# Kernel optimization log

Hardware: AMD Instinct MI355X
Metric: run time of the kernel (lower is better)

The kernel has to match this reference:

```python
import jax, jax.numpy as jnp
import numpy as np

N, HW, L = 16, 3136, 64
C_IN, C_OUT, D = 256, 512, 256


def setup_inputs() -> dict:
    key = jax.random.key(0)
    ks = jax.random.split(key, 8)
    # xavier-normal-ish scale for weights
    def xav(k, shape):
        fan_in, fan_out = shape[1], shape[0]
        std = (2.0 / (fan_in + fan_out)) ** 0.5
        return jax.random.normal(k, shape, dtype=jnp.float32) * std
    return {
        "x": jax.random.normal(ks[0], (N, HW, C_IN), dtype=jnp.float32),
        "t": jax.random.normal(ks[1], (N, L, D), dtype=jnp.float32),
        "W1": xav(ks[2], (D, C_IN)),      # linear1 weight (out,in), no bias
        "W2": xav(ks[3], (D, D)),         # linear2 weight, no bias
        "W3": xav(ks[4], (C_OUT, D)),     # linear3 weight
        "b3": jnp.zeros((C_OUT,), dtype=jnp.float32),
        "Wd": xav(ks[5], (C_OUT, C_IN)),  # downsample weight
        "bd": jnp.zeros((C_OUT,), dtype=jnp.float32),
    }


def reference(x, t, W1, W2, W3, b3, Wd, bd):
    # x: (N, HW, C_in), t: (N, L, D)
    x_q = jnp.einsum("npc,dc->npd", x, W1)          # (N, HW, D)
    t_q = jnp.einsum("nld,ed->nle", t, W2)          # (N, L, D)
    a = jnp.einsum("npd,nld->npl", x_q, t_q)        # unscaled QK^T (N, HW, L)
    a = jax.nn.softmax(a, axis=2)
    t3 = jnp.einsum("nld,od->nlo", t, W3) + b3      # (N, L, C_out)
    av = jnp.einsum("npl,nlo->npo", a, t3)          # (N, HW, C_out)
    x_ds = jnp.einsum("npc,oc->npo", x, Wd) + bd    # downsample residual
    return x_ds + av
```

## Files before the change

kernel.cpp:

```cpp
#include <hip/hip_runtime.h>


typedef unsigned short u16;
using half8 = __attribute__((ext_vector_type(8))) _Float16;
using f32x4 = __attribute__((ext_vector_type(4))) float;

__device__ __forceinline__ u16 f2h(float f) {
  _Float16 h = (_Float16)f;
  union { _Float16 h; u16 u; } cv; cv.h = h;
  return cv.u;
}

__device__ __forceinline__ f32x4 mfma16(half8 a, half8 b, f32x4 c) {
  return __builtin_amdgcn_mfma_f32_16x16x32_f16(a, b, c, 0, 0, 0);
}

__global__ __launch_bounds__(256) void reblock_kernel(
    const float* __restrict__ W1, const float* __restrict__ W2,
    const float* __restrict__ W3, const float* __restrict__ Wd,
    const float* __restrict__ t,
    u16* __restrict__ W1f, u16* __restrict__ W2f, u16* __restrict__ W3f,
    u16* __restrict__ Wdf, u16* __restrict__ tf) {
  int b = blockIdx.x, k = threadIdx.x;
  const float* src; u16* dst; int row;
  if (b < 256)       { src = W1; dst = W1f; row = b; }
  else if (b < 512)  { src = W2; dst = W2f; row = b - 256; }
  else if (b < 1024) { src = W3; dst = W3f; row = b - 512; }
  else if (b < 1536) { src = Wd; dst = Wdf; row = b - 1024; }
  else               { src = t;  dst = tf;  row = b - 1536; }
  float v = src[(size_t)row*256 + k];
  int flat = ((row >> 4)*8 + (k >> 5))*512 + ((k >> 3) & 3)*128 + (row & 15)*8 + (k & 7);
  dst[flat] = f2h(v);
}

__global__ __launch_bounds__(256) void tq_t3t_kernel(
    const u16* __restrict__ tf, const u16* __restrict__ W2f,
    const u16* __restrict__ W3f, const float* __restrict__ b3,
    u16* __restrict__ tqf, u16* __restrict__ t3f) {
  const int tid = threadIdx.x, w = tid >> 6, lane = tid & 63;
  const int quad = lane >> 4, l16 = lane & 15;
  const int b = blockIdx.x;

  if (b < 64) {
    const int n = b >> 2, eb = b & 3;
    const int gW2 = eb*4 + w;
    f32x4 acc[4];
    #pragma unroll
    for (int mt = 0; mt < 4; ++mt) acc[mt] = (f32x4){0.f, 0.f, 0.f, 0.f};
    #pragma unroll
    for (int kc = 0; kc < 8; ++kc) {
      half8 bf = *(const half8*)(W2f + (gW2*8 + kc)*512 + lane*8);
      #pragma unroll
      for (int mt = 0; mt < 4; ++mt) {
        half8 a = *(const half8*)(tf + ((n*4 + mt)*8 + kc)*512 + lane*8);
        acc[mt] = mfma16(a, bf, acc[mt]);
      }
    }
    #pragma unroll
    for (int mt = 0; mt < 4; ++mt)
      #pragma unroll
      for (int r = 0; r < 4; ++r) {
        int flat = ((n*4 + mt)*8 + eb*2 + (w >> 1))*512
                 + ((w & 1)*2 + (l16 >> 3))*128 + (quad*4 + r)*8 + (l16 & 7);
        tqf[flat] = f2h(acc[mt][r]);
      }
  } else {
    const int b2 = b - 64;
    const int n = b2 >> 3, ob = b2 & 7;
    const int gW3 = ob*4 + w;
    f32x4 acc[4];
    #pragma unroll
    for (int nt = 0; nt < 4; ++nt) acc[nt] = (f32x4){0.f, 0.f, 0.f, 0.f};
    #pragma unroll
    for (int kc = 0; kc < 8; ++kc) {
      half8 a = *(const half8*)(W3f + (gW3*8 + kc)*512 + lane*8);
      #pragma unroll
      for (int nt = 0; nt < 4; ++nt) {
        half8 bf = *(const half8*)(tf + ((n*4 + nt)*8 + kc)*512 + lane*8);
        acc[nt] = mfma16(a, bf, acc[nt]);
      }
    }
    #pragma unroll
    for (int nt = 0; nt < 4; ++nt)
      #pragma unroll
      for (int r = 0; r < 4; ++r) {
        int o = ob*64 + w*16 + quad*4 + r;
        int flat = ((n*32 + ob*4 + w)*2 + (nt >> 1))*512
                 + ((nt & 1)*2 + (l16 >> 3))*128 + (quad*4 + r)*8 + (l16 & 7);
        t3f[flat] = f2h(acc[nt][r] + b3[o]);
      }
  }
}

__global__ __launch_bounds__(512, 4) void main_kernel(
    const float* __restrict__ x, const u16* __restrict__ W1f,
    const u16* __restrict__ Wdf, const u16* __restrict__ tqf,
    const u16* __restrict__ t3f, const float* __restrict__ bd,
    float* __restrict__ out) {
  __shared__ __attribute__((aligned(16))) char smem[34816 + 17408];
  u16* xs   = (u16*)smem;
  u16* pool = (u16*)(smem + 34816);

  const int bid = blockIdx.x;
  const int n = bid / 49;
  const int pt = bid - n*49;
  const int m0 = pt * 64;
  const int tid = threadIdx.x, w = tid >> 6, lane = tid & 63;
  const int quad = lane >> 4, l16 = lane & 15;

  half8 w1a[8];
  {
    const u16* p = W1f + (size_t)w*8*512;
    #pragma unroll
    for (int kc = 0; kc < 8; ++kc) w1a[kc] = *(const half8*)(p + kc*512 + lane*8);
  }
  float bias[4];
  #pragma unroll
  for (int ot = 0; ot < 4; ++ot) bias[ot] = bd[w*64 + ot*16 + l16];

  {
    const float4* xg = (const float4*)(x + (size_t)(n*3136 + m0)*256);
    #pragma unroll
    for (int it = 0; it < 8; ++it) {
      int idx = it*512 + tid;
      int r = idx >> 6, c4 = idx & 63;
      float4 v = xg[idx];
      ushort4 u;
      u.x = f2h(v.x); u.y = f2h(v.y); u.z = f2h(v.z); u.w = f2h(v.w);
      *(ushort4*)(&xs[r*264 + c4*4]) = u;
    }
  }
  __syncthreads();

  f32x4 acc1[4];
  #pragma unroll
  for (int mt = 0; mt < 4; ++mt) acc1[mt] = (f32x4){0.f, 0.f, 0.f, 0.f};
  #pragma unroll
  for (int kc = 0; kc < 8; ++kc)
    #pragma unroll
    for (int mt = 0; mt < 4; ++mt) {
      half8 a = *(const half8*)(&xs[(mt*16 + l16)*264 + kc*32 + quad*8]);
      acc1[mt] = mfma16(a, w1a[kc], acc1[mt]);
    }
  #pragma unroll
  for (int mt = 0; mt < 4; ++mt)
    #pragma unroll
    for (int r = 0; r < 4; ++r)
      pool[(mt*16 + quad*4 + r)*136 + w*16 + l16] = f2h(acc1[mt][r]);
  __syncthreads();

  f32x4 acc2[4];
  #pragma unroll
  for (int lt = 0; lt < 4; ++lt) acc2[lt] = (f32x4){0.f, 0.f, 0.f, 0.f};
  f32x4 acc[4][4];
  #pragma unroll
  for (int mt = 0; mt < 4; ++mt)
    #pragma unroll
    for (int ot = 0; ot < 4; ++ot) acc[mt][ot] = (f32x4){0.f, 0.f, 0.f, 0.f};

  f32x4 acc1b[4];
  #pragma unroll
  for (int mt = 0; mt < 4; ++mt) acc1b[mt] = (f32x4){0.f, 0.f, 0.f, 0.f};
  {
    const u16* p = W1f + (size_t)(8 + w)*8*512;
    #pragma unroll
    for (int kc = 0; kc < 8; ++kc) {
      half8 bf = *(const half8*)(p + kc*512 + lane*8);
      #pragma unroll
      for (int mt = 0; mt < 4; ++mt) {
        half8 a = *(const half8*)(&xs[(mt*16 + l16)*264 + kc*32 + quad*8]);
        acc1b[mt] = mfma16(a, bf, acc1b[mt]);
      }
    }
  }
  if (w < 4) {
    #pragma unroll
    for (int k2 = 0; k2 < 4; ++k2) {
      half8 a = *(const half8*)(&pool[(w*16 + l16)*136 + k2*32 + quad*8]);
      #pragma unroll
      for (int lt = 0; lt < 4; ++lt) {
        half8 bf = *(const half8*)(tqf + ((n*4 + lt)*8 + 0*4 + k2)*512 + lane*8);
        acc2[lt] = mfma16(a, bf, acc2[lt]);
      }
    }
  }
  __syncthreads();
  #pragma unroll
  for (int mt = 0; mt < 4; ++mt)
    #pragma unroll
    for (int r = 0; r < 4; ++r)
      pool[(mt*16 + quad*4 + r)*136 + w*16 + l16] = f2h(acc1b[mt][r]);
  __syncthreads();

  if (w < 4) {
    #pragma unroll
    for (int k2 = 0; k2 < 4; ++k2) {
      half8 a = *(const half8*)(&pool[(w*16 + l16)*136 + k2*32 + quad*8]);
      #pragma unroll
      for (int lt = 0; lt < 4; ++lt) {
        half8 bf = *(const half8*)(tqf + ((n*4 + lt)*8 + 1*4 + k2)*512 + lane*8);
        acc2[lt] = mfma16(a, bf, acc2[lt]);
      }
    }
  }
  #pragma unroll
  for (int kc = 0; kc < 8; ++kc) {
    half8 a[4];
    #pragma unroll
    for (int mt = 0; mt < 4; ++mt)
      a[mt] = *(const half8*)(&xs[(mt*16 + l16)*264 + kc*32 + quad*8]);
    #pragma unroll
    for (int ot = 0; ot < 4; ++ot) {
      half8 bf = *(const half8*)(Wdf + ((w*4 + ot)*8 + kc)*512 + lane*8);
      #pragma unroll
      for (int mt = 0; mt < 4; ++mt) acc[mt][ot] = mfma16(a[mt], bf, acc[mt][ot]);
    }
  }
  __syncthreads();

  if (w < 4) {
    #pragma unroll
    for (int r = 0; r < 4; ++r) {
      float s0 = acc2[0][r], s1 = acc2[1][r], s2 = acc2[2][r], s3 = acc2[3][r];
      float mx = fmaxf(fmaxf(s0, s1), fmaxf(s2, s3));
      #pragma unroll
      for (int off = 8; off >= 1; off >>= 1) mx = fmaxf(mx, __shfl_xor(mx, off, 64));
      float e0 = __expf(s0 - mx), e1 = __expf(s1 - mx);
      float e2 = __expf(s2 - mx), e3 = __expf(s3 - mx);
      float s = e0 + e1 + e2 + e3;
      #pragma unroll
      for (int off = 8; off >= 1; off >>= 1) s += __shfl_xor(s, off, 64);
      float inv = 1.0f / s;
      int row = (w*16 + quad*4 + r)*72;
      pool[row +  0 + l16] = f2h(e0 * inv);
      pool[row + 16 + l16] = f2h(e1 * inv);
      pool[row + 32 + l16] = f2h(e2 * inv);
      pool[row + 48 + l16] = f2h(e3 * inv);
    }
  }
  __syncthreads();

  #pragma unroll
  for (int kc3 = 0; kc3 < 2; ++kc3) {
    half8 a[4];
    #pragma unroll
    for (int mt = 0; mt < 4; ++mt)
      a[mt] = *(const half8*)(&pool[(mt*16 + l16)*72 + kc3*32 + quad*8]);
    #pragma unroll
    for (int ot = 0; ot < 4; ++ot) {
      half8 bf = *(const half8*)(t3f + ((n*32 + w*4 + ot)*2 + kc3)*512 + lane*8);
      #pragma unroll
      for (int mt = 0; mt < 4; ++mt) acc[mt][ot] = mfma16(a[mt], bf, acc[mt][ot]);
    }
  }

  float* sc = (float*)smem + w*1088;
  #pragma unroll
  for (int mt = 0; mt < 4; ++mt) {
    #pragma unroll
    for (int ot = 0; ot < 4; ++ot)
      #pragma unroll
      for (int r = 0; r < 4; ++r)
        sc[(quad*4 + r)*68 + ot*16 + l16] = acc[mt][ot][r] + bias[ot];
    #pragma unroll
    for (int i = 0; i < 4; ++i) {
      float4 v = *(float4*)&sc[(i*4 + quad)*68 + l16*4];
      *(float4*)&out[(size_t)(n*3136 + m0 + mt*16 + i*4 + quad)*512 + w*64 + l16*4] = v;
    }
  }
}

extern "C" void kernel_launch(void* const* d_in, const int* in_sizes, int n_in,
                              void* d_out, int out_size, void* d_ws, size_t ws_size,
                              hipStream_t stream) {
  const float* x  = (const float*)d_in[0];
  const float* t  = (const float*)d_in[1];
  const float* W1 = (const float*)d_in[2];
  const float* W2 = (const float*)d_in[3];
  const float* W3 = (const float*)d_in[4];
  const float* b3 = (const float*)d_in[5];
  const float* Wd = (const float*)d_in[6];
  const float* bd = (const float*)d_in[7];
  float* out = (float*)d_out;

  char* ws = (char*)d_ws;
  u16* W1f = (u16*)(ws + 0);
  u16* W2f = (u16*)(ws + 131072);
  u16* W3f = (u16*)(ws + 262144);
  u16* Wdf = (u16*)(ws + 524288);
  u16* tf  = (u16*)(ws + 786432);
  u16* tqf = (u16*)(ws + 1310720);
  u16* t3f = (u16*)(ws + 1835008);

  hipLaunchKernelGGL(reblock_kernel, dim3(2560), dim3(256), 0, stream,
                     W1, W2, W3, Wd, t, W1f, W2f, W3f, Wdf, tf);
  hipLaunchKernelGGL(tq_t3t_kernel, dim3(192), dim3(256), 0, stream,
                     tf, W2f, W3f, b3, tqf, t3f);
  hipLaunchKernelGGL(main_kernel, dim3(784), dim3(512), 0, stream,
                     x, W1f, Wdf, tqf, t3f, bd, out);
}
```

Baseline: 196.2 us.

## Halve main kernel tile to 32 rows with 4 waves and split softmax

The main kernel now processes 32 pixel rows per block with 256 threads instead of 64 rows with 512, doubling the grid to 1568 blocks. Each wave computes two W1 column tiles and 128 output columns, done in two halves so fewer accumulators are live at once. The softmax over L is split across wave pairs and combined through a small shared buffer of partial max and sum values, so all waves take part instead of half. Output is stored straight from registers without the shared-memory staging pass. This gives more blocks and less shared memory per block, at the cost of less reuse of weight fragments per pixel, more global weight traffic, and uncoalesced output stores.

```diff
diff --git a/kernel.cpp b/kernel.cpp
--- a/kernel.cpp
+++ b/kernel.cpp
@@ -92,37 +92,41 @@
   }
 }
 
-__global__ __launch_bounds__(512, 4) void main_kernel(
+__global__ __launch_bounds__(256, 4) void main_kernel(
     const float* __restrict__ x, const u16* __restrict__ W1f,
     const u16* __restrict__ Wdf, const u16* __restrict__ tqf,
     const u16* __restrict__ t3f, const float* __restrict__ bd,
     float* __restrict__ out) {
-  __shared__ __attribute__((aligned(16))) char smem[34816 + 17408];
-  u16* xs   = (u16*)smem;
-  u16* pool = (u16*)(smem + 34816);
+  __shared__ __attribute__((aligned(16))) char smem[34816];
+  u16* xs  = (u16*)smem;
+  u16* xq0 = (u16*)(smem + 16896);
+  u16* xq1 = (u16*)(smem + 25600);
+  float* parts = (float*)(smem + 34304);
 
   const int bid = blockIdx.x;
-  const int n = bid / 49;
-  const int pt = bid - n*49;
-  const int m0 = pt * 64;
+  const int n  = bid / 98;
+  const int pt = bid - n*98;
+  const int m0 = pt * 32;
   const int tid = threadIdx.x, w = tid >> 6, lane = tid & 63;
   const int quad = lane >> 4, l16 = lane & 15;
+  const int rb = w & 1;
+  const int lh = w >> 1;
 
   half8 w1a[8];
   {
-    const u16* p = W1f + (size_t)w*8*512;
+    const u16* p = W1f + (size_t)(w*2)*8*512;
     #pragma unroll
     for (int kc = 0; kc < 8; ++kc) w1a[kc] = *(const half8*)(p + kc*512 + lane*8);
   }
-  float bias[4];
-  #pragma unroll
-  for (int ot = 0; ot < 4; ++ot) bias[ot] = bd[w*64 + ot*16 + l16];
+  float bias[8];
+  #pragma unroll
+  for (int og = 0; og < 8; ++og) bias[og] = bd[w*128 + og*16 + l16];
 
   {
     const float4* xg = (const float4*)(x + (size_t)(n*3136 + m0)*256);
     #pragma unroll
     for (int it = 0; it < 8; ++it) {
-      int idx = it*512 + tid;
+      int idx = it*256 + tid;
       int r = idx >> 6, c4 = idx & 63;
       float4 v = xg[idx];
       ushort4 u;
@@ -132,142 +136,187 @@
   }
   __syncthreads();
 
-  f32x4 acc1[4];
-  #pragma unroll
-  for (int mt = 0; mt < 4; ++mt) acc1[mt] = (f32x4){0.f, 0.f, 0.f, 0.f};
-  #pragma unroll
-  for (int kc = 0; kc < 8; ++kc)
-    #pragma unroll
-    for (int mt = 0; mt < 4; ++mt) {
-      half8 a = *(const half8*)(&xs[(mt*16 + l16)*264 + kc*32 + quad*8]);
-      acc1[mt] = mfma16(a, w1a[kc], acc1[mt]);
-    }
-  #pragma unroll
-  for (int mt = 0; mt < 4; ++mt)
-    #pragma unroll
-    for (int r = 0; r < 4; ++r)
-      pool[(mt*16 + quad*4 + r)*136 + w*16 + l16] = f2h(acc1[mt][r]);
-  __syncthreads();
-
-  f32x4 acc2[4];
-  #pragma unroll
-  for (int lt = 0; lt < 4; ++lt) acc2[lt] = (f32x4){0.f, 0.f, 0.f, 0.f};
-  f32x4 acc[4][4];
-  #pragma unroll
-  for (int mt = 0; mt < 4; ++mt)
+  f32x4 acc1[2][2];
+  #pragma unroll
+  for (int i = 0; i < 2; ++i)
+    #pragma unroll
+    for (int mt = 0; mt < 2; ++mt) acc1[i][mt] = (f32x4){0.f, 0.f, 0.f, 0.f};
+  {
+    const u16* p1 = W1f + (size_t)(w*2 + 1)*8*512;
+    #pragma unroll
+    for (int kc = 0; kc < 8; ++kc) {
+      half8 a0 = *(const half8*)(&xs[(l16)*264 + kc*32 + quad*8]);
+      half8 a1 = *(const half8*)(&xs[(16 + l16)*264 + kc*32 + quad*8]);
+      acc1[0][0] = mfma16(a0, w1a[kc], acc1[0][0]);
+      acc1[0][1] = mfma16(a1, w1a[kc], acc1[0][1]);
+      half8 bf = *(const half8*)(p1 + kc*512 + lane*8);
+      acc1[1][0] = mfma16(a0, bf, acc1[1][0]);
+      acc1[1][1] = mfma16(a1, bf, acc1[1][1]);
+    }
+  }
+  #pragma unroll
+  for (int i = 0; i < 2; ++i)
+    #pragma unroll
+    for (int mt = 0; mt < 2; ++mt)
+      #pragma unroll
+      for (int r = 0; r < 4; ++r)
+        xq0[(mt*16 + quad*4 + r)*136 + (w*2 + i)*16 + l16] = f2h(acc1[i][mt][r]);
+  __syncthreads();
+
+  f32x4 acc2[2];
+  acc2[0] = (f32x4){0.f, 0.f, 0.f, 0.f};
+  acc2[1] = (f32x4){0.f, 0.f, 0.f, 0.f};
+  #pragma unroll
+  for (int k2 = 0; k2 < 4; ++k2) {
+    half8 a = *(const half8*)(&xq0[(rb*16 + l16)*136 + k2*32 + quad*8]);
+    #pragma unroll
+    for (int j = 0; j < 2; ++j) {
+      half8 bf = *(const half8*)(tqf + ((size_t)(n*4 + lh*2 + j)*8 + k2)*512 + lane*8);
+      acc2[j] = mfma16(a, bf, acc2[j]);
+    }
+  }
+  {
+    f32x4 acc1b[2][2];
+    #pragma unroll
+    for (int i = 0; i < 2; ++i)
+      #pragma unroll
+      for (int mt = 0; mt < 2; ++mt) acc1b[i][mt] = (f32x4){0.f, 0.f, 0.f, 0.f};
+    const u16* pa = W1f + (size_t)(8 + w*2)*8*512;
+    const u16* pb = W1f + (size_t)(9 + w*2)*8*512;
+    #pragma unroll
+    for (int kc = 0; kc < 8; ++kc) {
+      half8 a0 = *(const half8*)(&xs[(l16)*264 + kc*32 + quad*8]);
+      half8 a1 = *(const half8*)(&xs[(16 + l16)*264 + kc*32 + quad*8]);
+      half8 bfA = *(const half8*)(pa + kc*512 + lane*8);
+      half8 bfB = *(const half8*)(pb + kc*512 + lane*8);
+      acc1b[0][0] = mfma16(a0, bfA, acc1b[0][0]);
+      acc1b[0][1] = mfma16(a1, bfA, acc1b[0][1]);
+      acc1b[1][0] = mfma16(a0, bfB, acc1b[1][0]);
+      acc1b[1][1] = mfma16(a1, bfB, acc1b[1][1]);
+    }
+    #pragma unroll
+    for (int i = 0; i < 2; ++i)
+      #pragma unroll
+      for (int mt = 0; mt < 2; ++mt)
+        #pragma unroll
+        for (int r = 0; r < 4; ++r)
+          xq1[(mt*16 + quad*4 + r)*136 + (w*2 + i)*16 + l16] = f2h(acc1b[i][mt][r]);
+  }
+  __syncthreads();
+
+  #pragma unroll
+  for (int k2 = 0; k2 < 4; ++k2) {
+    half8 a = *(const half8*)(&xq1[(rb*16 + l16)*136 + k2*32 + quad*8]);
+    #pragma unroll
+    for (int j = 0; j < 2; ++j) {
+      half8 bf = *(const half8*)(tqf + ((size_t)(n*4 + lh*2 + j)*8 + 4 + k2)*512 + lane*8);
+      acc2[j] = mfma16(a, bf, acc2[j]);
+    }
+  }
+  f32x4 acc[2][4];
+  #pragma unroll
+  for (int mt = 0; mt < 2; ++mt)
     #pragma unroll
     for (int ot = 0; ot < 4; ++ot) acc[mt][ot] = (f32x4){0.f, 0.f, 0.f, 0.f};
-
-  f32x4 acc1b[4];
-  #pragma unroll
-  for (int mt = 0; mt < 4; ++mt) acc1b[mt] = (f32x4){0.f, 0.f, 0.f, 0.f};
-  {
-    const u16* p = W1f + (size_t)(8 + w)*8*512;
-    #pragma unroll
-    for (int kc = 0; kc < 8; ++kc) {
-      half8 bf = *(const half8*)(p + kc*512 + lane*8);
-      #pragma unroll
-      for (int mt = 0; mt < 4; ++mt) {
-        half8 a = *(const half8*)(&xs[(mt*16 + l16)*264 + kc*32 + quad*8]);
-        acc1b[mt] = mfma16(a, bf, acc1b[mt]);
-      }
-    }
-  }
-  if (w < 4) {
-    #pragma unroll
-    for (int k2 = 0; k2 < 4; ++k2) {
-      half8 a = *(const half8*)(&pool[(w*16 + l16)*136 + k2*32 + quad*8]);
-      #pragma unroll
-      for (int lt = 0; lt < 4; ++lt) {
-        half8 bf = *(const half8*)(tqf + ((n*4 + lt)*8 + 0*4 + k2)*512 + lane*8);
-        acc2[lt] = mfma16(a, bf, acc2[lt]);
-      }
-    }
-  }
-  __syncthreads();
-  #pragma unroll
-  for (int mt = 0; mt < 4; ++mt)
-    #pragma unroll
-    for (int r = 0; r < 4; ++r)
-      pool[(mt*16 + quad*4 + r)*136 + w*16 + l16] = f2h(acc1b[mt][r]);
-  __syncthreads();
-
-  if (w < 4) {
-    #pragma unroll
-    for (int k2 = 0; k2 < 4; ++k2) {
-      half8 a = *(const half8*)(&pool[(w*16 + l16)*136 + k2*32 + quad*8]);
-      #pragma unroll
-      for (int lt = 0; lt < 4; ++lt) {
-        half8 bf = *(const half8*)(tqf + ((n*4 + lt)*8 + 1*4 + k2)*512 + lane*8);
-        acc2[lt] = mfma16(a, bf, acc2[lt]);
-      }
-    }
-  }
   #pragma unroll
   for (int kc = 0; kc < 8; ++kc) {
-    half8 a[4];
-    #pragma unroll
-    for (int mt = 0; mt < 4; ++mt)
-      a[mt] = *(const half8*)(&xs[(mt*16 + l16)*264 + kc*32 + quad*8]);
+    half8 a0 = *(const half8*)(&xs[(l16)*264 + kc*32 + quad*8]);
+    half8 a1 = *(const half8*)(&xs[(16 + l16)*264 + kc*32 + quad*8]);
     #pragma unroll
     for (int ot = 0; ot < 4; ++ot) {
-      half8 bf = *(const half8*)(Wdf + ((w*4 + ot)*8 + kc)*512 + lane*8);
-      #pragma unroll
-      for (int mt = 0; mt < 4; ++mt) acc[mt][ot] = mfma16(a[mt], bf, acc[mt][ot]);
-    }
-  }
-  __syncthreads();
-
-  if (w < 4) {
-    #pragma unroll
-    for (int r = 0; r < 4; ++r) {
-      float s0 = acc2[0][r], s1 = acc2[1][r], s2 = acc2[2][r], s3 = acc2[3][r];
-      float mx = fmaxf(fmaxf(s0, s1), fmaxf(s2, s3));
-      #pragma unroll
-      for (int off = 8; off >= 1; off >>= 1) mx = fmaxf(mx, __shfl_xor(mx, off, 64));
-      float e0 = __expf(s0 - mx), e1 = __expf(s1 - mx);
-      float e2 = __expf(s2 - mx), e3 = __expf(s3 - mx);
-      float s = e0 + e1 + e2 + e3;
-      #pragma unroll
-      for (int off = 8; off >= 1; off >>= 1) s += __shfl_xor(s, off, 64);
-      float inv = 1.0f / s;
-      int row = (w*16 + quad*4 + r)*72;
-      pool[row +  0 + l16] = f2h(e0 * inv);
-      pool[row + 16 + l16] = f2h(e1 * inv);
-      pool[row + 32 + l16] = f2h(e2 * inv);
-      pool[row + 48 + l16] = f2h(e3 * inv);
-    }
+      half8 bf = *(const half8*)(Wdf + ((size_t)(w*8 + ot)*8 + kc)*512 + lane*8);
+      acc[0][ot] = mfma16(a0, bf, acc[0][ot]);
+      acc[1][ot] = mfma16(a1, bf, acc[1][ot]);
+    }
+  }
+  float mx_[4], ps_[4], e0_[4], e1_[4];
+  #pragma unroll
+  for (int r = 0; r < 4; ++r) {
+    float s0 = acc2[0][r], s1 = acc2[1][r];
+    float mx = fmaxf(s0, s1);
+    #pragma unroll
+    for (int off = 8; off >= 1; off >>= 1) mx = fmaxf(mx, __shfl_xor(mx, off, 64));
+    float e0 = __expf(s0 - mx), e1 = __expf(s1 - mx);
+    float ps = e0 + e1;
+    #pragma unroll
+    for (int off = 8; off >= 1; off >>= 1) ps += __shfl_xor(ps, off, 64);
+    mx_[r] = mx; ps_[r] = ps; e0_[r] = e0; e1_[r] = e1;
+    if (l16 == 0) {
+      int pi = (rb*2 + lh)*16 + quad*4 + r;
+      parts[pi*2]     = mx;
+      parts[pi*2 + 1] = ps;
+    }
+  }
+  __syncthreads();
+
+  u16* aw = xq0;
+  #pragma unroll
+  for (int r = 0; r < 4; ++r) {
+    int pi = (rb*2 + (1 - lh))*16 + quad*4 + r;
+    float mxo = parts[pi*2], pso = parts[pi*2 + 1];
+    float g  = fmaxf(mx_[r], mxo);
+    float sA = __expf(mx_[r] - g), sB = __expf(mxo - g);
+    float inv = 1.0f / (ps_[r]*sA + pso*sB);
+    float scl = sA * inv;
+    int row = (rb*16 + quad*4 + r)*72;
+    aw[row + lh*32 + l16]      = f2h(e0_[r]*scl);
+    aw[row + lh*32 + 16 + l16] = f2h(e1_[r]*scl);
   }
   __syncthreads();
 
   #pragma unroll
   for (int kc3 = 0; kc3 < 2; ++kc3) {
-    half8 a[4];
-    #pragma unroll
-    for (int mt = 0; mt < 4; ++mt)
-      a[mt] = *(const half8*)(&pool[(mt*16 + l16)*72 + kc3*32 + quad*8]);
+    half8 a0 = *(const half8*)(&aw[(l16)*72 + kc3*32 + quad*8]);
+    half8 a1 = *(const half8*)(&aw[(16 + l16)*72 + kc3*32 + quad*8]);
     #pragma unroll
     for (int ot = 0; ot < 4; ++ot) {
-      half8 bf = *(const half8*)(t3f + ((n*32 + w*4 + ot)*2 + kc3)*512 + lane*8);
-      #pragma unroll
-      for (int mt = 0; mt < 4; ++mt) acc[mt][ot] = mfma16(a[mt], bf, acc[mt][ot]);
-    }
-  }
-
-  float* sc = (float*)smem + w*1088;
-  #pragma unroll
-  for (int mt = 0; mt < 4; ++mt) {
+      half8 bf = *(const half8*)(t3f + ((size_t)(n*32 + w*8 + ot)*2 + kc3)*512 + lane*8);
+      acc[0][ot] = mfma16(a0, bf, acc[0][ot]);
+      acc[1][ot] = mfma16(a1, bf, acc[1][ot]);
+    }
+  }
+  float* ob = out + (size_t)(n*3136 + m0)*512 + w*128;
+  #pragma unroll
+  for (int mt = 0; mt < 2; ++mt)
     #pragma unroll
     for (int ot = 0; ot < 4; ++ot)
       #pragma unroll
       for (int r = 0; r < 4; ++r)
-        sc[(quad*4 + r)*68 + ot*16 + l16] = acc[mt][ot][r] + bias[ot];
-    #pragma unroll
-    for (int i = 0; i < 4; ++i) {
-      float4 v = *(float4*)&sc[(i*4 + quad)*68 + l16*4];
-      *(float4*)&out[(size_t)(n*3136 + m0 + mt*16 + i*4 + quad)*512 + w*64 + l16*4] = v;
-    }
-  }
+        ob[(size_t)(mt*16 + quad*4 + r)*512 + ot*16 + l16] = acc[mt][ot][r] + bias[ot];
+
+  #pragma unroll
+  for (int mt = 0; mt < 2; ++mt)
+    #pragma unroll
+    for (int ot = 0; ot < 4; ++ot) acc[mt][ot] = (f32x4){0.f, 0.f, 0.f, 0.f};
+  #pragma unroll
+  for (int kc = 0; kc < 8; ++kc) {
+    half8 a0 = *(const half8*)(&xs[(l16)*264 + kc*32 + quad*8]);
+    half8 a1 = *(const half8*)(&xs[(16 + l16)*264 + kc*32 + quad*8]);
+    #pragma unroll
+    for (int ot = 0; ot < 4; ++ot) {
+      half8 bf = *(const half8*)(Wdf + ((size_t)(w*8 + 4 + ot)*8 + kc)*512 + lane*8);
+      acc[0][ot] = mfma16(a0, bf, acc[0][ot]);
+      acc[1][ot] = mfma16(a1, bf, acc[1][ot]);
+    }
+  }
+  #pragma unroll
+  for (int kc3 = 0; kc3 < 2; ++kc3) {
+    half8 a0 = *(const half8*)(&aw[(l16)*72 + kc3*32 + quad*8]);
+    half8 a1 = *(const half8*)(&aw[(16 + l16)*72 + kc3*32 + quad*8]);
+    #pragma unroll
+    for (int ot = 0; ot < 4; ++ot) {
+      half8 bf = *(const half8*)(t3f + ((size_t)(n*32 + w*8 + 4 + ot)*2 + kc3)*512 + lane*8);
+      acc[0][ot] = mfma16(a0, bf, acc[0][ot]);
+      acc[1][ot] = mfma16(a1, bf, acc[1][ot]);
+    }
+  }
+  #pragma unroll
+  for (int mt = 0; mt < 2; ++mt)
+    #pragma unroll
+    for (int ot = 0; ot < 4; ++ot)
+      #pragma unroll
+      for (int r = 0; r < 4; ++r)
+        ob[(size_t)(mt*16 + quad*4 + r)*512 + 64 + ot*16 + l16] = acc[mt][ot][r] + bias[4 + ot];
 }
 
 extern "C" void kernel_launch(void* const* d_in, const int* in_sizes, int n_in,
@@ -296,6 +345,6 @@
                      W1, W2, W3, Wd, t, W1f, W2f, W3f, Wdf, tf);
   hipLaunchKernelGGL(tq_t3t_kernel, dim3(192), dim3(256), 0, stream,
                      tf, W2f, W3f, b3, tqf, t3f);
-  hipLaunchKernelGGL(main_kernel, dim3(784), dim3(512), 0, stream,
+  hipLaunchKernelGGL(main_kernel, dim3(1568), dim3(256), 0, stream,
                      x, W1f, Wdf, tqf, t3f, bd, out);
 }
```

After: 213.0 us. +8.6%, slower.

## Fold W1 and W2 into one matrix so scores come straight from x

Applied to the files above, without the earlier changes.

Reassociates the score computation: precomputes G = W1^T W2 and M = t·G^T, so attention logits are x·M^T and the per-tile x_q projection (256-wide GEMM plus LDS round trips) is gone from the main kernel. The softmax is split across wave pairs, each handling half the L columns, with a cross-wave max/sum merge through shared memory. This removes a large block of MFMA work and several barriers per tile. In exchange the prep kernel does a naive scalar 256x256x256 product, and precision changes because G is rounded to fp16.

```diff
diff --git a/kernel.cpp b/kernel.cpp
--- a/kernel.cpp
+++ b/kernel.cpp
@@ -15,41 +15,49 @@
   return __builtin_amdgcn_mfma_f32_16x16x32_f16(a, b, c, 0, 0, 0);
 }
 
-__global__ __launch_bounds__(256) void reblock_kernel(
+__global__ __launch_bounds__(256) void prep_kernel(
     const float* __restrict__ W1, const float* __restrict__ W2,
     const float* __restrict__ W3, const float* __restrict__ Wd,
     const float* __restrict__ t,
-    u16* __restrict__ W1f, u16* __restrict__ W2f, u16* __restrict__ W3f,
-    u16* __restrict__ Wdf, u16* __restrict__ tf) {
+    u16* __restrict__ W3f, u16* __restrict__ Wdf, u16* __restrict__ tf,
+    u16* __restrict__ Gtf) {
   int b = blockIdx.x, k = threadIdx.x;
-  const float* src; u16* dst; int row;
-  if (b < 256)       { src = W1; dst = W1f; row = b; }
-  else if (b < 512)  { src = W2; dst = W2f; row = b - 256; }
-  else if (b < 1024) { src = W3; dst = W3f; row = b - 512; }
-  else if (b < 1536) { src = Wd; dst = Wdf; row = b - 1024; }
-  else               { src = t;  dst = tf;  row = b - 1536; }
-  float v = src[(size_t)row*256 + k];
-  int flat = ((row >> 4)*8 + (k >> 5))*512 + ((k >> 3) & 3)*128 + (row & 15)*8 + (k & 7);
-  dst[flat] = f2h(v);
-}
-
-__global__ __launch_bounds__(256) void tq_t3t_kernel(
-    const u16* __restrict__ tf, const u16* __restrict__ W2f,
+  if (b < 2048) {
+    const float* src; u16* dst; int row;
+    if (b < 512)       { src = W3; dst = W3f; row = b; }
+    else if (b < 1024) { src = Wd; dst = Wdf; row = b - 512; }
+    else               { src = t;  dst = tf;  row = b - 1024; }
+    float v = src[(size_t)row*256 + k];
+    int flat = ((row >> 4)*8 + (k >> 5))*512 + ((k >> 3) & 3)*128 + (row & 15)*8 + (k & 7);
+    dst[flat] = f2h(v);
+  } else {
+    int c = b - 2048;
+    float g = 0.f;
+    #pragma unroll 8
+    for (int d = 0; d < 256; ++d)
+      g = fmaf(W1[d*256 + c], W2[d*256 + k], g);
+    int flat = ((c >> 4)*8 + (k >> 5))*512 + ((k >> 3) & 3)*128 + (c & 15)*8 + (k & 7);
+    Gtf[flat] = f2h(g);
+  }
+}
+
+__global__ __launch_bounds__(256) void mt_t3_kernel(
+    const u16* __restrict__ tf, const u16* __restrict__ Gtf,
     const u16* __restrict__ W3f, const float* __restrict__ b3,
-    u16* __restrict__ tqf, u16* __restrict__ t3f) {
+    u16* __restrict__ mtf, u16* __restrict__ t3f) {
   const int tid = threadIdx.x, w = tid >> 6, lane = tid & 63;
   const int quad = lane >> 4, l16 = lane & 15;
   const int b = blockIdx.x;
 
   if (b < 64) {
     const int n = b >> 2, eb = b & 3;
-    const int gW2 = eb*4 + w;
+    const int gc = eb*4 + w;
     f32x4 acc[4];
     #pragma unroll
     for (int mt = 0; mt < 4; ++mt) acc[mt] = (f32x4){0.f, 0.f, 0.f, 0.f};
     #pragma unroll
     for (int kc = 0; kc < 8; ++kc) {
-      half8 bf = *(const half8*)(W2f + (gW2*8 + kc)*512 + lane*8);
+      half8 bf = *(const half8*)(Gtf + (gc*8 + kc)*512 + lane*8);
       #pragma unroll
       for (int mt = 0; mt < 4; ++mt) {
         half8 a = *(const half8*)(tf + ((n*4 + mt)*8 + kc)*512 + lane*8);
@@ -62,7 +70,7 @@
       for (int r = 0; r < 4; ++r) {
         int flat = ((n*4 + mt)*8 + eb*2 + (w >> 1))*512
                  + ((w & 1)*2 + (l16 >> 3))*128 + (quad*4 + r)*8 + (l16 & 7);
-        tqf[flat] = f2h(acc[mt][r]);
+        mtf[flat] = f2h(acc[mt][r]);
       }
   } else {
     const int b2 = b - 64;
@@ -93,27 +101,23 @@
 }
 
 __global__ __launch_bounds__(512, 4) void main_kernel(
-    const float* __restrict__ x, const u16* __restrict__ W1f,
-    const u16* __restrict__ Wdf, const u16* __restrict__ tqf,
-    const u16* __restrict__ t3f, const float* __restrict__ bd,
-    float* __restrict__ out) {
-  __shared__ __attribute__((aligned(16))) char smem[34816 + 17408];
-  u16* xs   = (u16*)smem;
-  u16* pool = (u16*)(smem + 34816);
+    const float* __restrict__ x, const u16* __restrict__ Wdf,
+    const u16* __restrict__ mtf, const u16* __restrict__ t3f,
+    const float* __restrict__ bd, float* __restrict__ out) {
+  __shared__ __attribute__((aligned(16))) char smem[44032];
+  u16* xs = (u16*)smem;
+  u16* aw = (u16*)(smem + 33792);
+  float* parts = (float*)(smem + 43008);
 
   const int bid = blockIdx.x;
-  const int n = bid / 49;
+  const int n  = bid / 49;
   const int pt = bid - n*49;
   const int m0 = pt * 64;
   const int tid = threadIdx.x, w = tid >> 6, lane = tid & 63;
   const int quad = lane >> 4, l16 = lane & 15;
-
-  half8 w1a[8];
-  {
-    const u16* p = W1f + (size_t)w*8*512;
-    #pragma unroll
-    for (int kc = 0; kc < 8; ++kc) w1a[kc] = *(const half8*)(p + kc*512 + lane*8);
-  }
+  const int rg = w & 3;
+  const int lp = w >> 2;
+
   float bias[4];
   #pragma unroll
   for (int ot = 0; ot < 4; ++ot) bias[ot] = bd[w*64 + ot*16 + l16];
@@ -132,77 +136,58 @@
   }
   __syncthreads();
 
-  f32x4 acc1[4];
-  #pragma unroll
-  for (int mt = 0; mt < 4; ++mt) acc1[mt] = (f32x4){0.f, 0.f, 0.f, 0.f};
-  #pragma unroll
-  for (int kc = 0; kc < 8; ++kc)
-    #pragma unroll
-    for (int mt = 0; mt < 4; ++mt) {
-      half8 a = *(const half8*)(&xs[(mt*16 + l16)*264 + kc*32 + quad*8]);
-      acc1[mt] = mfma16(a, w1a[kc], acc1[mt]);
-    }
+  f32x4 acc2[2];
+  acc2[0] = (f32x4){0.f, 0.f, 0.f, 0.f};
+  acc2[1] = (f32x4){0.f, 0.f, 0.f, 0.f};
+  #pragma unroll
+  for (int kc = 0; kc < 8; ++kc) {
+    half8 a = *(const half8*)(&xs[(rg*16 + l16)*264 + kc*32 + quad*8]);
+    #pragma unroll
+    for (int j = 0; j < 2; ++j) {
+      half8 bf = *(const half8*)(mtf + ((size_t)(n*4 + lp*2 + j)*8 + kc)*512 + lane*8);
+      acc2[j] = mfma16(a, bf, acc2[j]);
+    }
+  }
+
+  float mx_[4], ps_[4], e0_[4], e1_[4];
+  #pragma unroll
+  for (int r = 0; r < 4; ++r) {
+    float s0 = acc2[0][r], s1 = acc2[1][r];
+    float mx = fmaxf(s0, s1);
+    #pragma unroll
+    for (int off = 8; off >= 1; off >>= 1) mx = fmaxf(mx, __shfl_xor(mx, off, 64));
+    float e0 = __expf(s0 - mx), e1 = __expf(s1 - mx);
+    float ps = e0 + e1;
+    #pragma unroll
+    for (int off = 8; off >= 1; off >>= 1) ps += __shfl_xor(ps, off, 64);
+    mx_[r] = mx; ps_[r] = ps; e0_[r] = e0; e1_[r] = e1;
+    if (l16 == 0) {
+      int row = rg*16 + quad*4 + r;
+      parts[(row*2 + lp)*2]     = mx;
+      parts[(row*2 + lp)*2 + 1] = ps;
+    }
+  }
+  __syncthreads();
+
+  #pragma unroll
+  for (int r = 0; r < 4; ++r) {
+    int row = rg*16 + quad*4 + r;
+    float mxo = parts[(row*2 + (1 - lp))*2];
+    float pso = parts[(row*2 + (1 - lp))*2 + 1];
+    float g  = fmaxf(mx_[r], mxo);
+    float sA = __expf(mx_[r] - g), sB = __expf(mxo - g);
+    float inv = 1.0f / (ps_[r]*sA + pso*sB);
+    float scl = sA * inv;
+    aw[row*72 + (lp*2)*16 + l16]     = f2h(e0_[r]*scl);
+    aw[row*72 + (lp*2 + 1)*16 + l16] = f2h(e1_[r]*scl);
+  }
+  __syncthreads();
+
+  f32x4 acc[4][4];
   #pragma unroll
   for (int mt = 0; mt < 4; ++mt)
     #pragma unroll
-    for (int r = 0; r < 4; ++r)
-      pool[(mt*16 + quad*4 + r)*136 + w*16 + l16] = f2h(acc1[mt][r]);
-  __syncthreads();
-
-  f32x4 acc2[4];
-  #pragma unroll
-  for (int lt = 0; lt < 4; ++lt) acc2[lt] = (f32x4){0.f, 0.f, 0.f, 0.f};
-  f32x4 acc[4][4];
-  #pragma unroll
-  for (int mt = 0; mt < 4; ++mt)
-    #pragma unroll
     for (int ot = 0; ot < 4; ++ot) acc[mt][ot] = (f32x4){0.f, 0.f, 0.f, 0.f};
-
-  f32x4 acc1b[4];
-  #pragma unroll
-  for (int mt = 0; mt < 4; ++mt) acc1b[mt] = (f32x4){0.f, 0.f, 0.f, 0.f};
-  {
-    const u16* p = W1f + (size_t)(8 + w)*8*512;
-    #pragma unroll
-    for (int kc = 0; kc < 8; ++kc) {
-      half8 bf = *(const half8*)(p + kc*512 + lane*8);
-      #pragma unroll
-      for (int mt = 0; mt < 4; ++mt) {
-        half8 a = *(const half8*)(&xs[(mt*16 + l16)*264 + kc*32 + quad*8]);
-        acc1b[mt] = mfma16(a, bf, acc1b[mt]);
-      }
-    }
-  }
-  if (w < 4) {
-    #pragma unroll
-    for (int k2 = 0; k2 < 4; ++k2) {
-      half8 a = *(const half8*)(&pool[(w*16 + l16)*136 + k2*32 + quad*8]);
-      #pragma unroll
-      for (int lt = 0; lt < 4; ++lt) {
-        half8 bf = *(const half8*)(tqf + ((n*4 + lt)*8 + 0*4 + k2)*512 + lane*8);
-        acc2[lt] = mfma16(a, bf, acc2[lt]);
-      }
-    }
-  }
-  __syncthreads();
-  #pragma unroll
-  for (int mt = 0; mt < 4; ++mt)
-    #pragma unroll
-    for (int r = 0; r < 4; ++r)
-      pool[(mt*16 + quad*4 + r)*136 + w*16 + l16] = f2h(acc1b[mt][r]);
-  __syncthreads();
-
-  if (w < 4) {
-    #pragma unroll
-    for (int k2 = 0; k2 < 4; ++k2) {
-      half8 a = *(const half8*)(&pool[(w*16 + l16)*136 + k2*32 + quad*8]);
-      #pragma unroll
-      for (int lt = 0; lt < 4; ++lt) {
-        half8 bf = *(const half8*)(tqf + ((n*4 + lt)*8 + 1*4 + k2)*512 + lane*8);
-        acc2[lt] = mfma16(a, bf, acc2[lt]);
-      }
-    }
-  }
   #pragma unroll
   for (int kc = 0; kc < 8; ++kc) {
     half8 a[4];
@@ -211,48 +196,25 @@
       a[mt] = *(const half8*)(&xs[(mt*16 + l16)*264 + kc*32 + quad*8]);
     #pragma unroll
     for (int ot = 0; ot < 4; ++ot) {
-      half8 bf = *(const half8*)(Wdf + ((w*4 + ot)*8 + kc)*512 + lane*8);
+      half8 bf = *(const half8*)(Wdf + ((size_t)(w*4 + ot)*8 + kc)*512 + lane*8);
       #pragma unroll
       for (int mt = 0; mt < 4; ++mt) acc[mt][ot] = mfma16(a[mt], bf, acc[mt][ot]);
     }
   }
-  __syncthreads();
-
-  if (w < 4) {
-    #pragma unroll
-    for (int r = 0; r < 4; ++r) {
-      float s0 = acc2[0][r], s1 = acc2[1][r], s2 = acc2[2][r], s3 = acc2[3][r];
-      float mx = fmaxf(fmaxf(s0, s1), fmaxf(s2, s3));
-      #pragma unroll
-      for (int off = 8; off >= 1; off >>= 1) mx = fmaxf(mx, __shfl_xor(mx, off, 64));
-      float e0 = __expf(s0 - mx), e1 = __expf(s1 - mx);
-      float e2 = __expf(s2 - mx), e3 = __expf(s3 - mx);
-      float s = e0 + e1 + e2 + e3;
-      #pragma unroll
-      for (int off = 8; off >= 1; off >>= 1) s += __shfl_xor(s, off, 64);
-      float inv = 1.0f / s;
-      int row = (w*16 + quad*4 + r)*72;
-      pool[row +  0 + l16] = f2h(e0 * inv);
-      pool[row + 16 + l16] = f2h(e1 * inv);
-      pool[row + 32 + l16] = f2h(e2 * inv);
-      pool[row + 48 + l16] = f2h(e3 * inv);
-    }
-  }
-  __syncthreads();
-
   #pragma unroll
   for (int kc3 = 0; kc3 < 2; ++kc3) {
     half8 a[4];
     #pragma unroll
     for (int mt = 0; mt < 4; ++mt)
-      a[mt] = *(const half8*)(&pool[(mt*16 + l16)*72 + kc3*32 + quad*8]);
+      a[mt] = *(const half8*)(&aw[(mt*16 + l16)*72 + kc3*32 + quad*8]);
     #pragma unroll
     for (int ot = 0; ot < 4; ++ot) {
-      half8 bf = *(const half8*)(t3f + ((n*32 + w*4 + ot)*2 + kc3)*512 + lane*8);
+      half8 bf = *(const half8*)(t3f + ((size_t)(n*32 + w*4 + ot)*2 + kc3)*512 + lane*8);
       #pragma unroll
       for (int mt = 0; mt < 4; ++mt) acc[mt][ot] = mfma16(a[mt], bf, acc[mt][ot]);
     }
   }
+  __syncthreads();
 
   float* sc = (float*)smem + w*1088;
   #pragma unroll
@@ -284,18 +246,17 @@
   float* out = (float*)d_out;
 
   char* ws = (char*)d_ws;
-  u16* W1f = (u16*)(ws + 0);
-  u16* W2f = (u16*)(ws + 131072);
-  u16* W3f = (u16*)(ws + 262144);
-  u16* Wdf = (u16*)(ws + 524288);
-  u16* tf  = (u16*)(ws + 786432);
-  u16* tqf = (u16*)(ws + 1310720);
-  u16* t3f = (u16*)(ws + 1835008);
-
-  hipLaunchKernelGGL(reblock_kernel, dim3(2560), dim3(256), 0, stream,
-                     W1, W2, W3, Wd, t, W1f, W2f, W3f, Wdf, tf);
-  hipLaunchKernelGGL(tq_t3t_kernel, dim3(192), dim3(256), 0, stream,
-                     tf, W2f, W3f, b3, tqf, t3f);
+  u16* W3f = (u16*)(ws + 0);
+  u16* Wdf = (u16*)(ws + 262144);
+  u16* tf  = (u16*)(ws + 524288);
+  u16* Gtf = (u16*)(ws + 1048576);
+  u16* mtf = (u16*)(ws + 1179648);
+  u16* t3f = (u16*)(ws + 1703936);
+
+  hipLaunchKernelGGL(prep_kernel, dim3(2304), dim3(256), 0, stream,
+                     W1, W2, W3, Wd, t, W3f, Wdf, tf, Gtf);
+  hipLaunchKernelGGL(mt_t3_kernel, dim3(192), dim3(256), 0, stream,
+                     tf, Gtf, W3f, b3, mtf, t3f);
   hipLaunchKernelGGL(main_kernel, dim3(784), dim3(512), 0, stream,
-                     x, W1f, Wdf, tqf, t3f, bd, out);
-}
+                     x, Wdf, mtf, t3f, bd, out);
+}
```

New measurement: 205.7 us. 4.8% more time.
